# Kernel optimization log

Measured on AMD Instinct MI355X. Metric: run time of the kernel, lower is better.

## Reference

```python
import jax, jax.numpy as jnp
import numpy as np

B, S, D, H, L, NS = 16, 1024, 512, 8, 4, 4
HD = D // H            # head dim = 64
FF = 4 * D             # dim_feedforward
VOCAB = 64
OUT = 64


def _ln(x, g, b, eps=1e-5):
    m = jnp.mean(x, -1, keepdims=True)
    v = jnp.var(x, -1, keepdims=True)
    return (x - m) * jax.lax.rsqrt(v + eps) * g + b


def setup_inputs() -> dict:
    key = jax.random.key(0)
    ks = iter(jax.random.split(key, 40))
    def w(shape, s=0.02):
        return jax.random.normal(next(ks), shape, jnp.float32) * s
    return {
        "x_batch": jax.random.randint(next(ks), (B, S), 0, VOCAB),
        "context_batch": jax.random.normal(next(ks), (B, 2), jnp.float32),
        "specialist_ids": jax.random.randint(next(ks), (B,), 0, NS),
        "emb_table": w((VOCAB, D), 1.0),
        "wqkv": w((L, D, 3 * D)), "bqkv": jnp.zeros((L, 3 * D), jnp.float32),
        "wo": w((L, D, D)), "bo": jnp.zeros((L, D), jnp.float32),
        "ln1_g": jnp.ones((L, D), jnp.float32), "ln1_b": jnp.zeros((L, D), jnp.float32),
        "w1": w((L, D, FF)), "b1": jnp.zeros((L, FF), jnp.float32),
        "w2": w((L, FF, D)), "b2": jnp.zeros((L, D), jnp.float32),
        "ln2_g": jnp.ones((L, D), jnp.float32), "ln2_b": jnp.zeros((L, D), jnp.float32),
        "ctx_w": w((2, D)), "ctx_b": jnp.zeros((D,), jnp.float32),
        "ca_wq": w((D, D)), "ca_bq": jnp.zeros((D,), jnp.float32),
        "ca_wk": w((D, D)), "ca_bk": jnp.zeros((D,), jnp.float32),
        "ca_wv": w((D, D)), "ca_bv": jnp.zeros((D,), jnp.float32),
        "ca_wo": w((D, D)), "ca_bo": jnp.zeros((D,), jnp.float32),
        "pred_w": w((NS, D, OUT)), "pred_b": jnp.zeros((NS, OUT), jnp.float32),
        "act_w": w((NS, D, OUT)), "act_b": jnp.zeros((NS, OUT), jnp.float32),
    }


def _forward(x_batch, context_batch, specialist_ids, emb_table,
             wqkv, bqkv, wo, bo, ln1_g, ln1_b, w1, b1, w2, b2, ln2_g, ln2_b,
             ctx_w, ctx_b, ca_wq, ca_bq, ca_wk, ca_bk, ca_wv, ca_bv, ca_wo, ca_bo,
             pred_w, pred_b, act_w, act_b):
    b, s = x_batch.shape
    x = emb_table[x_batch]                                   # [B,S,D]
    causal = jnp.triu(jnp.full((s, s), -jnp.inf, jnp.float32), 1)
    scale = 1.0 / np.sqrt(HD)
    nlayers = wqkv.shape[0]
    for i in range(nlayers):  # post-LN TransformerEncoderLayer (torch default)
        qkv = x @ wqkv[i] + bqkv[i]
        q, k, v = jnp.split(qkv, 3, axis=-1)
        q = q.reshape(b, s, H, HD)
        k = k.reshape(b, s, H, HD)
        v = v.reshape(b, s, H, HD)
        scores = jnp.einsum('bqhd,bkhd->bhqk', q, k) * scale + causal
        a = jax.nn.softmax(scores, axis=-1)
        o = jnp.einsum('bhqk,bkhd->bqhd', a, v).reshape(b, s, -1)
        x = _ln(x + o @ wo[i] + bo[i], ln1_g[i], ln1_b[i])
        ff = jax.nn.relu(x @ w1[i] + b1[i]) @ w2[i] + b2[i]
        x = _ln(x + ff, ln2_g[i], ln2_b[i])
    # single-token cross attention: kv comes from projected context
    ctx = (context_batch @ ctx_w + ctx_b)[:, None, :]        # [B,1,D]
    q = (x @ ca_wq + ca_bq).reshape(b, s, H, HD)
    k = (ctx @ ca_wk + ca_bk).reshape(b, 1, H, HD)
    v = (ctx @ ca_wv + ca_bv).reshape(b, 1, H, HD)
    sc = jnp.einsum('bqhd,bkhd->bhqk', q, k) * scale         # [B,H,S,1]
    a = jax.nn.softmax(sc, axis=-1)                          # all ones (kv_len=1)
    o = jnp.einsum('bhqk,bkhd->bqhd', a, v).reshape(b, s, -1)
    latent = o @ ca_wo + ca_bo                               # no residual, as in source
    last = latent[:, -1, :]                                  # [B,D]
    # specialist dispatch: gather per-sample expert weights, batched GEMV
    pred = jnp.einsum('bd,bdo->bo', last, pred_w[specialist_ids]) + pred_b[specialist_ids]
    act = jnp.einsum('bd,bdo->bo', last, act_w[specialist_ids]) + act_b[specialist_ids]
    return pred, act


def reference(x_batch, context_batch, specialist_ids, emb_table,
              wqkv, bqkv, wo, bo, ln1_g, ln1_b, w1, b1, w2, b2, ln2_g, ln2_b,
              ctx_w, ctx_b, ca_wq, ca_bq, ca_wk, ca_bk, ca_wv, ca_bv, ca_wo, ca_bo,
              pred_w, pred_b, act_w, act_b):
    return _forward(x_batch, context_batch, specialist_ids, emb_table,
                    wqkv, bqkv, wo, bo, ln1_g, ln1_b, w1, b1, w2, b2, ln2_g, ln2_b,
                    ctx_w, ctx_b, ca_wq, ca_bq, ca_wk, ca_bk, ca_wv, ca_bv, ca_wo, ca_bo,
                    pred_w, pred_b, act_w, act_b)
```

## Files before the change

### kernel.cpp

```cpp
#include <hip/hip_runtime.h>
#include <hip/hip_bf16.h>


#define DD 512
#define BB 16
#define OO 64

__global__ __launch_bounds__(1024) void k_fused(
    const float* __restrict__ cb,
    const float* __restrict__ cw,
    const float* __restrict__ cbias,
    const float* __restrict__ wv,
    const float* __restrict__ bv,
    const float* __restrict__ wo,
    const float* __restrict__ bo,
    const int*   __restrict__ sid,
    const float* __restrict__ pw,
    const float* __restrict__ pb,
    const float* __restrict__ aw,
    const float* __restrict__ ab,
    float*       __restrict__ out) {
  __shared__ float ctx_s[DD];
  __shared__ float buf_s[DD];
  __shared__ float red_s[1024];

  const int b   = blockIdx.x;
  const int tid = threadIdx.x;

  if (tid < DD) {
    const float c0 = cb[2 * b], c1 = cb[2 * b + 1];
    ctx_s[tid] = fmaf(c0, cw[tid], fmaf(c1, cw[DD + tid], cbias[tid]));
  }
  __syncthreads();

  {
    const int j = tid & (DD - 1);
    const int h = tid >> 9;
    float acc = h ? 0.0f : bv[j];
    const int d0 = h * (DD / 2);
#pragma unroll 8
    for (int d = 0; d < DD / 2; ++d)
      acc = fmaf(ctx_s[d0 + d], wv[(d0 + d) * DD + j], acc);
    red_s[tid] = acc;
  }
  __syncthreads();
  if (tid < DD) buf_s[tid] = red_s[tid] + red_s[tid + DD];
  __syncthreads();

  {
    const int j = tid & (DD - 1);
    const int h = tid >> 9;
    float acc = h ? 0.0f : bo[j];
    const int d0 = h * (DD / 2);
#pragma unroll 8
    for (int d = 0; d < DD / 2; ++d)
      acc = fmaf(buf_s[d0 + d], wo[(d0 + d) * DD + j], acc);
    red_s[tid] = acc;
  }
  __syncthreads();
  if (tid < DD) ctx_s[tid] = red_s[tid] + red_s[tid + DD];
  __syncthreads();

  {
    const int oi   = tid & 127;
    const int part = tid >> 7;
    const int half = oi >> 6;
    const int o    = oi & 63;
    const int s    = sid[b];
    const float* w    = half ? aw : pw;
    const float* bias = half ? ab : pb;
    float acc = (part == 0) ? bias[s * OO + o] : 0.0f;
    const int d0 = part * (DD / 8);
#pragma unroll 8
    for (int d = 0; d < DD / 8; ++d)
      acc = fmaf(ctx_s[d0 + d], w[(s * DD + d0 + d) * OO + o], acc);
    red_s[tid] = acc;
  }
  __syncthreads();
  if (tid < 128) {
    float acc = 0.0f;
#pragma unroll
    for (int p = 0; p < 8; ++p) acc += red_s[tid + 128 * p];
    const int half = tid >> 6, o = tid & 63;
    out[half * (BB * OO) + b * OO + o] = acc;
  }
}

extern "C" void kernel_launch(void* const* d_in, const int* in_sizes, int n_in,
                              void* d_out, int out_size, void* d_ws, size_t ws_size,
                              hipStream_t stream) {
  k_fused<<<BB, 1024, 0, stream>>>(
      reinterpret_cast<const float*>(d_in[1]),
      reinterpret_cast<const float*>(d_in[16]),
      reinterpret_cast<const float*>(d_in[17]),
      reinterpret_cast<const float*>(d_in[22]),
      reinterpret_cast<const float*>(d_in[23]),
      reinterpret_cast<const float*>(d_in[24]),
      reinterpret_cast<const float*>(d_in[25]),
      reinterpret_cast<const int*>(d_in[2]),
      reinterpret_cast<const float*>(d_in[26]),
      reinterpret_cast<const float*>(d_in[27]),
      reinterpret_cast<const float*>(d_in[28]),
      reinterpret_cast<const float*>(d_in[29]),
      reinterpret_cast<float*>(d_out));
}
```

Measured before the change: 161.2 us.

## Split fused per-batch GEMV chain into three batched tiled kernels

Replaces a single 16-block kernel, where each block reads the full V and O weight matrices for one sample, with three kernels. The first two tile the weight matrix across 64 blocks and compute all 16 batch rows per weight element in registers, writing split-K partials to workspace. A third kernel reduces those partials and runs the specialist head. This is meant to remove the 16x redundant weight traffic and the low block count, in exchange for two extra launches and partial sums round-tripping through global memory.

```diff
diff --git a/kernel.cpp b/kernel.cpp
--- a/kernel.cpp
+++ b/kernel.cpp
@@ -5,102 +5,148 @@
 #define DD 512
 #define BB 16
 #define OO 64
+#define NC 8
 
-__global__ __launch_bounds__(1024) void k_fused(
-    const float* __restrict__ cb,
-    const float* __restrict__ cw,
-    const float* __restrict__ cbias,
-    const float* __restrict__ wv,
-    const float* __restrict__ bv,
-    const float* __restrict__ wo,
-    const float* __restrict__ bo,
-    const int*   __restrict__ sid,
-    const float* __restrict__ pw,
-    const float* __restrict__ pb,
-    const float* __restrict__ aw,
-    const float* __restrict__ ab,
-    float*       __restrict__ out) {
-  __shared__ float ctx_s[DD];
-  __shared__ float buf_s[DD];
-  __shared__ float red_s[1024];
+__global__ __launch_bounds__(256) void k1_v(
+    const float* __restrict__ cb, const float* __restrict__ cw,
+    const float* __restrict__ cbias, const float* __restrict__ wv,
+    float* __restrict__ vpart) {
+  __shared__ float cs[BB * 64];
+  __shared__ float red[4 * BB * 64];
+  const int tid = threadIdx.x;
+  const int jb = blockIdx.x & 7, db = blockIdx.x >> 3;
+  const int d0 = db * 64, j0 = jb * 64;
 
-  const int b   = blockIdx.x;
-  const int tid = threadIdx.x;
-
-  if (tid < DD) {
-    const float c0 = cb[2 * b], c1 = cb[2 * b + 1];
-    ctx_s[tid] = fmaf(c0, cw[tid], fmaf(c1, cw[DD + tid], cbias[tid]));
+  for (int idx = tid; idx < BB * 64; idx += 256) {
+    const int b = idx >> 6, d = idx & 63;
+    cs[idx] = fmaf(cb[2 * b], cw[d0 + d],
+               fmaf(cb[2 * b + 1], cw[DD + d0 + d], cbias[d0 + d]));
   }
   __syncthreads();
 
-  {
-    const int j = tid & (DD - 1);
-    const int h = tid >> 9;
-    float acc = h ? 0.0f : bv[j];
-    const int d0 = h * (DD / 2);
-#pragma unroll 8
-    for (int d = 0; d < DD / 2; ++d)
-      acc = fmaf(ctx_s[d0 + d], wv[(d0 + d) * DD + j], acc);
-    red_s[tid] = acc;
+  const int j = tid & 63, dsub = tid >> 6;
+  float acc[BB];
+#pragma unroll
+  for (int b = 0; b < BB; ++b) acc[b] = 0.f;
+  float wr[16];
+#pragma unroll
+  for (int i = 0; i < 16; ++i)
+    wr[i] = wv[(d0 + dsub * 16 + i) * DD + j0 + j];
+#pragma unroll
+  for (int i = 0; i < 16; ++i) {
+    const int d = dsub * 16 + i;
+#pragma unroll
+    for (int b = 0; b < BB; ++b) acc[b] = fmaf(cs[b * 64 + d], wr[i], acc[b]);
+  }
+#pragma unroll
+  for (int b = 0; b < BB; ++b) red[dsub * (BB * 64) + b * 64 + j] = acc[b];
+  __syncthreads();
+  for (int idx = tid; idx < BB * 64; idx += 256) {
+    float s = red[idx] + red[idx + BB * 64] + red[idx + 2 * BB * 64] + red[idx + 3 * BB * 64];
+    const int b = idx >> 6, jj = idx & 63;
+    vpart[(db * BB + b) * DD + j0 + jj] = s;
+  }
+}
+
+__global__ __launch_bounds__(256) void k2_o(
+    const float* __restrict__ bv, const float* __restrict__ wo,
+    const float* __restrict__ vpart, float* __restrict__ lpart) {
+  __shared__ float vs[BB * 64];
+  __shared__ float red[4 * BB * 64];
+  const int tid = threadIdx.x;
+  const int jb = blockIdx.x & 7, db = blockIdx.x >> 3;
+  const int d0 = db * 64, j0 = jb * 64;
+
+  for (int idx = tid; idx < BB * 64; idx += 256) {
+    const int b = idx >> 6, d = idx & 63;
+    float s = bv[d0 + d];
+#pragma unroll
+    for (int c = 0; c < NC; ++c) s += vpart[(c * BB + b) * DD + d0 + d];
+    vs[idx] = s;
   }
   __syncthreads();
-  if (tid < DD) buf_s[tid] = red_s[tid] + red_s[tid + DD];
+
+  const int j = tid & 63, dsub = tid >> 6;
+  float acc[BB];
+#pragma unroll
+  for (int b = 0; b < BB; ++b) acc[b] = 0.f;
+  float wr[16];
+#pragma unroll
+  for (int i = 0; i < 16; ++i)
+    wr[i] = wo[(d0 + dsub * 16 + i) * DD + j0 + j];
+#pragma unroll
+  for (int i = 0; i < 16; ++i) {
+    const int d = dsub * 16 + i;
+#pragma unroll
+    for (int b = 0; b < BB; ++b) acc[b] = fmaf(vs[b * 64 + d], wr[i], acc[b]);
+  }
+#pragma unroll
+  for (int b = 0; b < BB; ++b) red[dsub * (BB * 64) + b * 64 + j] = acc[b];
+  __syncthreads();
+  for (int idx = tid; idx < BB * 64; idx += 256) {
+    float s = red[idx] + red[idx + BB * 64] + red[idx + 2 * BB * 64] + red[idx + 3 * BB * 64];
+    const int b = idx >> 6, jj = idx & 63;
+    lpart[(db * BB + b) * DD + j0 + jj] = s;
+  }
+}
+
+__global__ __launch_bounds__(512) void k3_head(
+    const float* __restrict__ bo, const float* __restrict__ lpart,
+    const int* __restrict__ sid,
+    const float* __restrict__ pw, const float* __restrict__ pb,
+    const float* __restrict__ aw, const float* __restrict__ ab,
+    float* __restrict__ out) {
+  __shared__ float ls[DD];
+  __shared__ float red[8 * OO];
+  const int tid = threadIdx.x;
+  const int b = blockIdx.x & 15, half = blockIdx.x >> 4;
+
+  for (int d = tid; d < DD; d += 512) {
+    float s = bo[d];
+#pragma unroll
+    for (int c = 0; c < NC; ++c) s += lpart[(c * BB + b) * DD + d];
+    ls[d] = s;
+  }
   __syncthreads();
 
-  {
-    const int j = tid & (DD - 1);
-    const int h = tid >> 9;
-    float acc = h ? 0.0f : bo[j];
-    const int d0 = h * (DD / 2);
-#pragma unroll 8
-    for (int d = 0; d < DD / 2; ++d)
-      acc = fmaf(buf_s[d0 + d], wo[(d0 + d) * DD + j], acc);
-    red_s[tid] = acc;
-  }
+  const int s = sid[b];
+  const int o = tid & 63, dsub = tid >> 6;
+  const float* w = (half ? aw : pw) + (s * DD + dsub * 64) * OO + o;
+  float acc = 0.f;
+#pragma unroll 16
+  for (int i = 0; i < 64; ++i)
+    acc = fmaf(ls[dsub * 64 + i], w[i * OO], acc);
+  red[dsub * OO + o] = acc;
   __syncthreads();
-  if (tid < DD) ctx_s[tid] = red_s[tid] + red_s[tid + DD];
-  __syncthreads();
-
-  {
-    const int oi   = tid & 127;
-    const int part = tid >> 7;
-    const int half = oi >> 6;
-    const int o    = oi & 63;
-    const int s    = sid[b];
-    const float* w    = half ? aw : pw;
-    const float* bias = half ? ab : pb;
-    float acc = (part == 0) ? bias[s * OO + o] : 0.0f;
-    const int d0 = part * (DD / 8);
-#pragma unroll 8
-    for (int d = 0; d < DD / 8; ++d)
-      acc = fmaf(ctx_s[d0 + d], w[(s * DD + d0 + d) * OO + o], acc);
-    red_s[tid] = acc;
-  }
-  __syncthreads();
-  if (tid < 128) {
-    float acc = 0.0f;
+  if (tid < OO) {
+    float a = (half ? ab : pb)[s * OO + tid];
 #pragma unroll
-    for (int p = 0; p < 8; ++p) acc += red_s[tid + 128 * p];
-    const int half = tid >> 6, o = tid & 63;
-    out[half * (BB * OO) + b * OO + o] = acc;
+    for (int p = 0; p < 8; ++p) a += red[p * OO + tid];
+    out[half * (BB * OO) + b * OO + tid] = a;
   }
 }
 
 extern "C" void kernel_launch(void* const* d_in, const int* in_sizes, int n_in,
                               void* d_out, int out_size, void* d_ws, size_t ws_size,
                               hipStream_t stream) {
-  k_fused<<<BB, 1024, 0, stream>>>(
-      reinterpret_cast<const float*>(d_in[1]),
-      reinterpret_cast<const float*>(d_in[16]),
-      reinterpret_cast<const float*>(d_in[17]),
-      reinterpret_cast<const float*>(d_in[22]),
-      reinterpret_cast<const float*>(d_in[23]),
-      reinterpret_cast<const float*>(d_in[24]),
-      reinterpret_cast<const float*>(d_in[25]),
-      reinterpret_cast<const int*>(d_in[2]),
-      reinterpret_cast<const float*>(d_in[26]),
-      reinterpret_cast<const float*>(d_in[27]),
-      reinterpret_cast<const float*>(d_in[28]),
-      reinterpret_cast<const float*>(d_in[29]),
-      reinterpret_cast<float*>(d_out));
+  const float* cb    = reinterpret_cast<const float*>(d_in[1]);
+  const int*   sid   = reinterpret_cast<const int*>(d_in[2]);
+  const float* cw    = reinterpret_cast<const float*>(d_in[16]);
+  const float* cbias = reinterpret_cast<const float*>(d_in[17]);
+  const float* wv    = reinterpret_cast<const float*>(d_in[22]);
+  const float* bv    = reinterpret_cast<const float*>(d_in[23]);
+  const float* wo    = reinterpret_cast<const float*>(d_in[24]);
+  const float* bo    = reinterpret_cast<const float*>(d_in[25]);
+  const float* pw    = reinterpret_cast<const float*>(d_in[26]);
+  const float* pb    = reinterpret_cast<const float*>(d_in[27]);
+  const float* aw    = reinterpret_cast<const float*>(d_in[28]);
+  const float* ab    = reinterpret_cast<const float*>(d_in[29]);
+
+  float* vpart = reinterpret_cast<float*>(d_ws);
+  float* lpart = vpart + NC * BB * DD;
+
+  k1_v   <<<64, 256, 0, stream>>>(cb, cw, cbias, wv, vpart);
+  k2_o   <<<64, 256, 0, stream>>>(bv, wo, vpart, lpart);
+  k3_head<<<32, 512, 0, stream>>>(bo, lpart, sid, pw, pb, aw, ab,
+                                  reinterpret_cast<float*>(d_out));
 }
```

Measured after the change: 144.1 us. 1.12x faster.
